# Performance work log

Hardware: AMD Instinct MI355X
Metric: run time of the kernel (lower is better)

## Reference

```python
import jax, jax.numpy as jnp
import numpy as np

B, N, D, H, S = 64, 1000, 512, 8, 20
DK = D // H
TANH_CLIP = 10.0
NEG = -1e9


def setup_inputs() -> dict:
    key = jax.random.key(0)
    k1, k2, k3, k4, k5 = jax.random.split(key, 5)
    embeddings = jax.random.normal(k1, (B, N, D), dtype=jnp.float32)
    q = jax.random.normal(k2, (B, S, D), dtype=jnp.float32)
    # action_mask: True = feasible. Ensure at least one feasible node per row.
    action_mask = jax.random.bernoulli(k3, 0.5, (B, S, N))
    action_mask = action_mask.at[:, :, 0].set(True)
    W_kvl = jax.random.normal(k4, (D, 3 * D), dtype=jnp.float32) * (1.0 / np.sqrt(D))
    W_out = jax.random.normal(k5, (D, D), dtype=jnp.float32) * (1.0 / np.sqrt(D))
    return {"embeddings": embeddings, "q": q, "action_mask": action_mask,
            "W_kvl": W_kvl, "W_out": W_out}


def reference(embeddings, q, action_mask, W_kvl, W_out):
    # _precompute: project node embeddings into glimpse K, V and logit K
    kvl = jnp.einsum('bnd,de->bne', embeddings, W_kvl)  # [B,N,3D]
    glimpse_k, glimpse_v, logit_k = jnp.split(kvl, 3, axis=-1)
    # dynamic embedding is zero (StaticEmbedding for TSP)

    mask = ~action_mask  # True = infeasible, shape [B,S,N]

    # multi-head glimpse attention
    qh = q.reshape(B, S, H, DK)
    kh = glimpse_k.reshape(B, N, H, DK)
    vh = glimpse_v.reshape(B, N, H, DK)
    compat = jnp.einsum('bshd,bnhd->bhsn', qh, kh) / np.sqrt(DK)
    compat = jnp.where(mask[:, None, :, :], NEG, compat)
    attn = jax.nn.softmax(compat, axis=-1)
    heads = jnp.einsum('bhsn,bnhd->bshd', attn, vh).reshape(B, S, D)
    glimpse = jnp.einsum('bsd,de->bse', heads, W_out)  # [B,S,D]

    # pointer logits against logit_k, tanh clipping, mask, log-softmax
    logits = jnp.einsum('bsd,bnd->bsn', glimpse, logit_k) / np.sqrt(D)
    logits = TANH_CLIP * jnp.tanh(logits)
    logits = jnp.where(mask, NEG, logits)
    log_p = jax.nn.log_softmax(logits, axis=-1)  # [B,S,N]

    # rearrange 'b s l -> (s b) l'
    return jnp.swapaxes(log_p, 0, 1).reshape(S * B, N)
```

## Files before the change

### kernel.cpp

```cpp
#include <hip/hip_runtime.h>

#define BB 64
#define NN 1000
#define NP 1024
#define DD 512
#define HH 8
#define SS 20
#define NEGV -1e9f

typedef float v4f __attribute__((ext_vector_type(4)));
typedef short v8s __attribute__((ext_vector_type(8)));
typedef int   v8i __attribute__((ext_vector_type(8)));
typedef int   v4i __attribute__((ext_vector_type(4)));
typedef unsigned char uchar;
typedef unsigned long long ulong_t;

static __device__ __forceinline__ short f2bf(float f) {
    unsigned u = __builtin_bit_cast(unsigned, f);
    u = (u + 0x7fffu + ((u >> 16) & 1u)) >> 16;
    return (short)u;
}
static __device__ __forceinline__ float bf2f(short s) {
    unsigned u = ((unsigned)(unsigned short)s) << 16;
    return __builtin_bit_cast(float, u);
}
static __device__ __forceinline__ uchar f2fp8(float f) {
    return (uchar)(__builtin_amdgcn_cvt_pk_fp8_f32(f, 0.f, 0, false) & 0xff);
}

static __device__ __forceinline__ void gld16(const void* g, void* l) {
    __builtin_amdgcn_global_load_lds(
        (const __attribute__((address_space(1))) void*)(g),
        (__attribute__((address_space(3))) void*)(l),
        16, 0, 0);
}

__global__ void prep(const float* __restrict__ Wkvl, uchar* __restrict__ Wt8,
                     const float* __restrict__ Wout, short* __restrict__ Wot,
                     const float* __restrict__ emb, int* __restrict__ emb8) {
    __shared__ float t[32][33];
    int bid = blockIdx.x, tid = threadIdx.x;
    if (bid < 768) {
        int c0 = (bid % 48) * 32, r0 = (bid / 48) * 32;
        int x = tid & 31, y = tid >> 5;
        for (int k = 0; k < 32; k += 8)
            t[y + k][x] = Wkvl[(long)(r0 + y + k) * 1536 + c0 + x];
        __syncthreads();
        for (int k = 0; k < 32; k += 8)
            Wt8[(long)(c0 + y + k) * 512 + r0 + x] = f2fp8(t[x][y + k]);
    } else if (bid < 1024) {
        int bb = bid - 768;
        int c0 = (bb & 15) * 32, r0 = (bb >> 4) * 32;
        int x = tid & 31, y = tid >> 5;
        for (int k = 0; k < 32; k += 8)
            t[y + k][x] = Wout[(long)(r0 + y + k) * 512 + c0 + x];
        __syncthreads();
        for (int k = 0; k < 32; k += 8)
            Wot[(long)(c0 + y + k) * 512 + r0 + x] = f2bf(t[x][y + k]);
    } else {
        int i = (bid - 1024) * 256 + tid;
        long o = (long)i * 8;
        v4f a = *(const v4f*)(emb + o);
        v4f b = *(const v4f*)(emb + o + 4);
        int lo = __builtin_amdgcn_cvt_pk_fp8_f32(a.x, a.y, 0, false);
        lo = __builtin_amdgcn_cvt_pk_fp8_f32(a.z, a.w, lo, true);
        int hi = __builtin_amdgcn_cvt_pk_fp8_f32(b.x, b.y, 0, false);
        hi = __builtin_amdgcn_cvt_pk_fp8_f32(b.z, b.w, hi, true);
        int2 r; r.x = lo; r.y = hi;
        *(int2*)(emb8 + i * 2) = r;
    }
}

__global__ __launch_bounds__(512) void gemm_kvl(const uchar* __restrict__ emb8,
                                                const uchar* __restrict__ Wt8,
                                                uchar* __restrict__ kvl8) {
    extern __shared__ __align__(16) uchar smem[];
    uchar* As0 = smem;
    uchar* Bs0 = smem + 32768;
    int tid = threadIdx.x;
    int id = blockIdx.x;
    int wgid = (id & 7) * 750 + (id >> 3);
    int m_idx = wgid / 12, n_idx = wgid - m_idx * 12;
    int m0 = m_idx * 128, n0 = n_idx * 128;
    int wid = tid >> 6, lane = tid & 63, quad = lane >> 4, l16 = lane & 15;
    int wm = wid & 1, wn = wid >> 1;
    const uchar* Ag = emb8 + (long)m0 * 512;
    const uchar* Bg = Wt8 + (long)n0 * 512;
    int rsub = lane >> 3;
    int kc = ((lane & 7) ^ rsub) * 16;

    v4f acc[4][2] = {};

    auto stageAB = [&](int bi, int kk) {
        #pragma unroll
        for (int p = 0; p < 2; ++p) {
            int rl = wid * 16 + p * 8;
            gld16(Ag + (long)(rl + rsub) * 512 + kk + kc, As0 + bi * 16384 + rl * 128);
        }
        #pragma unroll
        for (int p = 0; p < 2; ++p) {
            int rl = wid * 16 + p * 8;
            gld16(Bg + (long)(rl + rsub) * 512 + kk + kc, Bs0 + bi * 16384 + rl * 128);
        }
    };
    auto ldfrag = [&](const uchar* base, int row) -> v8i {
        int c0 = (quad * 2) ^ (row & 7);
        v4i lo = *(const v4i*)(base + row * 128 + c0 * 16);
        v4i hi = *(const v4i*)(base + row * 128 + (c0 ^ 1) * 16);
        return __builtin_shufflevector(lo, hi, 0, 1, 2, 3, 4, 5, 6, 7);
    };

    stageAB(0, 0);
    stageAB(1, 128);
    asm volatile("s_waitcnt vmcnt(4)" ::: "memory");
    __builtin_amdgcn_s_barrier();
    __builtin_amdgcn_sched_barrier(0);

    v8i af[4], bf[2];
    #pragma unroll
    for (int t = 0; t < 4; ++t) {
        int cur = t & 1;
        const uchar* ab = As0 + cur * 16384;
        const uchar* bb = Bs0 + cur * 16384;
        #pragma unroll
        for (int i = 0; i < 4; ++i) af[i] = ldfrag(ab, wm * 64 + i * 16 + l16);
        #pragma unroll
        for (int j = 0; j < 2; ++j) bf[j] = ldfrag(bb, wn * 32 + j * 16 + l16);
        __builtin_amdgcn_s_setprio(1);
        #pragma unroll
        for (int i = 0; i < 4; ++i)
            acc[i][0] = __builtin_amdgcn_mfma_scale_f32_16x16x128_f8f6f4(
                af[i], bf[0], acc[i][0], 0, 0, 0, 0x7f7f7f7f, 0, 0x7f7f7f7f);
        __builtin_amdgcn_s_setprio(0);
        asm volatile("s_waitcnt lgkmcnt(0)" ::: "memory");
        __builtin_amdgcn_s_barrier();
        if (t < 2) stageAB(cur, (t + 2) * 128);
        __builtin_amdgcn_s_setprio(1);
        #pragma unroll
        for (int i = 0; i < 4; ++i)
            acc[i][1] = __builtin_amdgcn_mfma_scale_f32_16x16x128_f8f6f4(
                af[i], bf[1], acc[i][1], 0, 0, 0, 0x7f7f7f7f, 0, 0x7f7f7f7f);
        __builtin_amdgcn_s_setprio(0);
        if (t < 3) {
            if (t < 2) asm volatile("s_waitcnt vmcnt(4)" ::: "memory");
            else       asm volatile("s_waitcnt vmcnt(0)" ::: "memory");
            __builtin_amdgcn_s_barrier();
            __builtin_amdgcn_sched_barrier(0);
        }
    }
    __syncthreads();

    short* rp = (short*)smem;
    short* r = rp + wid * (16 * 40);
    int nw = n0 + wn * 32;
    #pragma unroll
    for (int i = 0; i < 4; ++i) {
        #pragma unroll
        for (int jj = 0; jj < 2; ++jj)
            #pragma unroll
            for (int rr = 0; rr < 4; ++rr)
                r[(quad * 4 + rr) * 40 + jj * 16 + l16] = f2bf(acc[i][jj][rr]);
        {
            int rowl = lane >> 2;
            int colc = (lane & 3) * 8;
            v8s val = *(const v8s*)(r + rowl * 40 + colc);
            int lo = __builtin_amdgcn_cvt_pk_fp8_f32(bf2f(val[0]), bf2f(val[1]), 0, false);
            lo = __builtin_amdgcn_cvt_pk_fp8_f32(bf2f(val[2]), bf2f(val[3]), lo, true);
            int hi = __builtin_amdgcn_cvt_pk_fp8_f32(bf2f(val[4]), bf2f(val[5]), 0, false);
            hi = __builtin_amdgcn_cvt_pk_fp8_f32(bf2f(val[6]), bf2f(val[7]), hi, true);
            int2 st; st.x = lo; st.y = hi;
            *(int2*)(kvl8 + (long)(m0 + wm * 64 + i * 16 + rowl) * 1536 +
                     nw + colc) = st;
        }
    }
}

__global__ void pack_kv(const uchar* __restrict__ kvl8, uchar* __restrict__ Kf,
                        uchar* __restrict__ Vf) {
    int bh = blockIdx.x, b = bh >> 3, h = bh & 7;
    int g = blockIdx.y;
    __shared__ uchar Kl[64][72];
    __shared__ uchar VT[64][72];
    int tid = threadIdx.x;
    int node_l = tid >> 2, chunk = (tid & 3) * 16;
    int gn = g * 64 + node_l;
    int ncl = gn < NN ? gn : NN - 1;
    const uchar* rowp = kvl8 + ((long)b * NN + ncl) * 1536 + h * 64;
    *(v4i*)&Kl[node_l][chunk] = *(const v4i*)(rowp + chunk);
    {
        const uchar* vp = rowp + 512 + chunk;
        ulong_t v0 = *(const ulong_t*)(vp);
        ulong_t v1 = *(const ulong_t*)(vp + 8);
        uchar* b0p = (uchar*)&v0; uchar* b1p = (uchar*)&v1;
        #pragma unroll
        for (int j = 0; j < 8; ++j) VT[chunk + j][node_l] = b0p[j];
        #pragma unroll
        for (int j = 0; j < 8; ++j) VT[chunk + 8 + j][node_l] = b1p[j];
    }
    __syncthreads();
    int wid = tid >> 6, lane = tid & 63, l16 = lane & 15, quad = lane >> 4;
    #pragma unroll
    for (int ks = 0; ks < 2; ++ks) {
        ulong_t frag = *(const ulong_t*)&Kl[wid * 16 + l16][ks * 32 + quad * 8];
        *(ulong_t*)(Kf + (((long)bh * 64 + g * 4 + wid) * 2 + ks) * 512 + lane * 8) = frag;
    }
    #pragma unroll
    for (int sub = 0; sub < 2; ++sub) {
        ulong_t frag = *(const ulong_t*)&VT[wid * 16 + l16][sub * 32 + quad * 8];
        *(ulong_t*)(Vf + (((long)bh * 4 + wid) * 32 + g * 2 + sub) * 512 + lane * 8) = frag;
    }
}

#define CST 1036
__global__ __launch_bounds__(512) void attn_fused(const float* __restrict__ q,
                                                  const uchar* __restrict__ Kf,
                                                  const uchar* __restrict__ Vf,
                                                  const int* __restrict__ mask,
                                                  float* __restrict__ heads) {
    int b = blockIdx.x, h = blockIdx.y;
    __shared__ __align__(16) uchar qs[32 * 72];
    __shared__ __align__(16) short cmp[SS * CST];
    int tid = threadIdx.x, wid = tid >> 6, lane = tid & 63, quad = lane >> 4, l16 = lane & 15;
    for (int i = tid; i < 32 * 64; i += 512) {
        int row = i >> 6, col = i & 63;
        float v = (row < SS) ? q[((long)b * SS + row) * DD + h * 64 + col] : 0.f;
        qs[row * 72 + col] = f2fp8(v);
    }
    __syncthreads();
    long af[2][2];
    #pragma unroll
    for (int mt = 0; mt < 2; ++mt)
        #pragma unroll
        for (int ks = 0; ks < 2; ++ks)
            af[mt][ks] = *(const long*)(qs + (mt * 16 + l16) * 72 + ks * 32 + quad * 8);
    const uchar* kfb = Kf + ((long)(b * HH + h) * 64) * 1024;
    for (int t = 0; t < 8; ++t) {
        int nt = wid * 8 + t;
        long b0 = *(const long*)(kfb + (long)nt * 1024 + lane * 8);
        long b1 = *(const long*)(kfb + (long)nt * 1024 + 512 + lane * 8);
        #pragma unroll
        for (int mt = 0; mt < 2; ++mt) {
            v4f a = {};
            a = __builtin_amdgcn_mfma_f32_16x16x32_fp8_fp8(af[mt][0], b0, a, 0, 0, 0);
            a = __builtin_amdgcn_mfma_f32_16x16x32_fp8_fp8(af[mt][1], b1, a, 0, 0, 0);
            #pragma unroll
            for (int r = 0; r < 4; ++r) {
                int s = mt * 16 + quad * 4 + r;
                if (s < SS) cmp[s * CST + nt * 16 + l16] = f2bf(a[r] * 0.125f);
            }
        }
    }
    __syncthreads();
    for (int s = wid; s < SS; s += 8) {
        const int* mr = mask + ((long)b * SS + s) * NN;
        float x[16];
        float mx = NEGV;
        #pragma unroll
        for (int i = 0; i < 16; ++i) {
            int n = lane + 64 * i;
            float v = bf2f(cmp[s * CST + n]);
            bool feas = (n < NN) && (mr[n < NN ? n : 0] != 0);
            x[i] = feas ? v : NEGV;
            mx = fmaxf(mx, x[i]);
        }
        for (int off = 32; off; off >>= 1) mx = fmaxf(mx, __shfl_xor(mx, off));
        float sum = 0.f;
        #pragma unroll
        for (int i = 0; i < 16; ++i) { x[i] = __expf(x[i] - mx); sum += x[i]; }
        for (int off = 32; off; off >>= 1) sum += __shfl_xor(sum, off);
        float inv = 1.0f / sum;
        uchar* pr = (uchar*)cmp + (long)s * (CST * 2);
        #pragma unroll
        for (int i = 0; i < 16; ++i) pr[lane + 64 * i] = f2fp8(x[i] * inv);
    }
    __syncthreads();
    int mt = wid & 1, dt = wid >> 1;
    int srow = mt * 16 + l16; if (srow > SS - 1) srow = SS - 1;
    const uchar* ap = (const uchar*)cmp + (long)srow * (CST * 2) + quad * 8;
    const uchar* vfb = Vf + (((long)(b * HH + h) * 4 + dt) * 32) * 512;
    v4f a0 = {}, a1 = {}, a2 = {}, a3 = {};
    for (int k0s = 0; k0s < 32; k0s += 4) {
        a0 = __builtin_amdgcn_mfma_f32_16x16x32_fp8_fp8(
            *(const long*)(ap + k0s * 32),
            *(const long*)(vfb + (long)k0s * 512 + lane * 8), a0, 0, 0, 0);
        a1 = __builtin_amdgcn_mfma_f32_16x16x32_fp8_fp8(
            *(const long*)(ap + (k0s + 1) * 32),
            *(const long*)(vfb + (long)(k0s + 1) * 512 + lane * 8), a1, 0, 0, 0);
        a2 = __builtin_amdgcn_mfma_f32_16x16x32_fp8_fp8(
            *(const long*)(ap + (k0s + 2) * 32),
            *(const long*)(vfb + (long)(k0s + 2) * 512 + lane * 8), a2, 0, 0, 0);
        a3 = __builtin_amdgcn_mfma_f32_16x16x32_fp8_fp8(
            *(const long*)(ap + (k0s + 3) * 32),
            *(const long*)(vfb + (long)(k0s + 3) * 512 + lane * 8), a3, 0, 0, 0);
    }
    v4f accv = (a0 + a1) + (a2 + a3);
    #pragma unroll
    for (int r = 0; r < 4; ++r) {
        int s = mt * 16 + quad * 4 + r;
        if (s < SS)
            heads[((long)b * SS + s) * DD + h * 64 + dt * 16 + l16] = accv[r];
    }
}

__global__ __launch_bounds__(256) void out_proj(const float* __restrict__ heads,
                                                const short* __restrict__ Wot,
                                                float* __restrict__ glimpse) {
    __shared__ __align__(16) short As[64 * 40], Bs[64 * 40];
    int tid = threadIdx.x;
    int m0 = blockIdx.x * 64, n0 = blockIdx.y * 64;
    int wid = tid >> 6, lane = tid & 63, quad = lane >> 4, l16 = lane & 15;
    int wm = wid & 1, wn = wid >> 1;
    int arow = tid >> 3, akol = (tid & 7) * 4;
    int brow = tid >> 2, bkol = (tid & 3) * 8;
    v4f acc[2][2] = {};
    for (int kk = 0; kk < 512; kk += 32) {
        #pragma unroll
        for (int p = 0; p < 2; ++p) {
            int r = arow + p * 32;
            v4f a = *(const v4f*)(heads + (long)(m0 + r) * 512 + kk + akol);
            short4 s4;
            s4.x = f2bf(a.x); s4.y = f2bf(a.y); s4.z = f2bf(a.z); s4.w = f2bf(a.w);
            *(short4*)(As + r * 40 + akol) = s4;
        }
        *(uint4*)(Bs + brow * 40 + bkol) =
            *(const uint4*)(Wot + (long)(n0 + brow) * 512 + kk + bkol);
        __syncthreads();
        #pragma unroll
        for (int i = 0; i < 2; ++i) {
            v8s af = *(const v8s*)(As + (wm * 32 + i * 16 + l16) * 40 + quad * 8);
            #pragma unroll
            for (int j = 0; j < 2; ++j) {
                v8s bf = *(const v8s*)(Bs + (wn * 32 + j * 16 + l16) * 40 + quad * 8);
                acc[i][j] = __builtin_amdgcn_mfma_f32_16x16x32_bf16(af, bf, acc[i][j], 0, 0, 0);
            }
        }
        __syncthreads();
    }
    #pragma unroll
    for (int i = 0; i < 2; ++i)
        #pragma unroll
        for (int j = 0; j < 2; ++j)
            #pragma unroll
            for (int r = 0; r < 4; ++r)
                glimpse[(long)(m0 + wm * 32 + i * 16 + quad * 4 + r) * 512 +
                        n0 + wn * 32 + j * 16 + l16] = acc[i][j][r];
}

__global__ __launch_bounds__(256) void ptr_logits(const float* __restrict__ glimpse,
                                                  const uchar* __restrict__ kvl8,
                                                  float* __restrict__ logits) {
    int b = blockIdx.x, g = blockIdx.y;
    __shared__ __align__(16) uchar Gs[32 * 520];
    int tid = threadIdx.x;
    #pragma unroll
    for (int it = 0; it < 16; ++it) {
        int e = it * 1024 + tid * 4;
        int row = e >> 9, col = e & 511;
        int pk = 0;
        if (row < SS) {
            v4f a = *(const v4f*)(glimpse + ((long)b * SS + row) * 512 + col);
            pk = __builtin_amdgcn_cvt_pk_fp8_f32(a.x, a.y, 0, false);
            pk = __builtin_amdgcn_cvt_pk_fp8_f32(a.z, a.w, pk, true);
        }
        *(int*)(Gs + row * 520 + col) = pk;
    }
    __syncthreads();
    int wid = tid >> 6, lane = tid & 63, quad = lane >> 4, l16 = lane & 15;
    const float scale = 0.04419417382415922f;
    int nt = g * 4 + wid;
    int n = nt * 16 + l16;
    int ncl = n < NN ? n : NN - 1;
    const uchar* kp = kvl8 + ((long)b * NN + ncl) * 1536 + 1024 + quad * 8;
    v4f acc[2] = {};
    for (int k = 0; k < 16; ++k) {
        long bfr = *(const long*)(kp + k * 32);
        #pragma unroll
        for (int m = 0; m < 2; ++m) {
            long afr = *(const long*)(Gs + (m * 16 + l16) * 520 + k * 32 + quad * 8);
            acc[m] = __builtin_amdgcn_mfma_f32_16x16x32_fp8_fp8(afr, bfr, acc[m], 0, 0, 0);
        }
    }
    #pragma unroll
    for (int m = 0; m < 2; ++m)
        #pragma unroll
        for (int r = 0; r < 4; ++r) {
            int s = m * 16 + quad * 4 + r;
            if (s < SS)
                logits[((long)b * SS + s) * NP + nt * 16 + l16] = acc[m][r] * scale;
        }
}

__global__ __launch_bounds__(256) void logsoftmax_out(const float* __restrict__ logits,
                                                      const int* __restrict__ mask,
                                                      float* __restrict__ out) {
    int row = blockIdx.x;
    int b = row / SS, s = row % SS;
    int tid = threadIdx.x;
    __shared__ float red[8];
    int n0 = tid * 4;
    v4f v = *(const v4f*)(logits + (long)row * NP + n0);
    const int* mr = mask + (long)row * NN;
    float x[4];
    float mx = NEGV;
    #pragma unroll
    for (int j = 0; j < 4; ++j) {
        int n = n0 + j;
        float t = 10.f * tanhf(v[j]);
        bool feas = (n < NN) && (mr[n < NN ? n : 0] != 0);
        x[j] = feas ? t : NEGV;
        mx = fmaxf(mx, x[j]);
    }
    for (int off = 32; off; off >>= 1) mx = fmaxf(mx, __shfl_xor(mx, off));
    int wid = tid >> 6, lane = tid & 63;
    if (lane == 0) red[wid] = mx;
    __syncthreads();
    mx = fmaxf(fmaxf(red[0], red[1]), fmaxf(red[2], red[3]));
    float sum = 0.f;
    #pragma unroll
    for (int j = 0; j < 4; ++j) sum += __expf(x[j] - mx);
    for (int off = 32; off; off >>= 1) sum += __shfl_xor(sum, off);
    __syncthreads();
    if (lane == 0) red[4 + wid] = sum;
    __syncthreads();
    sum = red[4] + red[5] + red[6] + red[7];
    float lse = mx + __logf(sum);
    float* orow = out + ((long)s * BB + b) * NN;
    #pragma unroll
    for (int j = 0; j < 4; ++j) {
        int n = n0 + j;
        if (n < NN) orow[n] = x[j] - lse;
    }
}

extern "C" void kernel_launch(void* const* d_in, const int* in_sizes, int n_in,
                              void* d_out, int out_size, void* d_ws, size_t ws_size,
                              hipStream_t stream) {
    const float* emb  = (const float*)d_in[0];
    const float* q    = (const float*)d_in[1];
    const int*   mask = (const int*)d_in[2];
    const float* Wkvl = (const float*)d_in[3];
    const float* Wout = (const float*)d_in[4];
    float* out = (float*)d_out;

    char* ws = (char*)d_ws;
    uchar* kvl8    = (uchar*)ws; ws += (size_t)64000 * 1536;
    uchar* Vf      = (uchar*)ws; ws += (size_t)512 * 64 * NP;
    uchar* Wt8     = (uchar*)ws; ws += (size_t)1536 * 512;
    uchar* emb8    = (uchar*)ws; ws += (size_t)64000 * 512;
    short* Wot     = (short*)ws; ws += (size_t)512 * 512 * 2;
    float* heads   = (float*)ws; ws += (size_t)BB * SS * DD * 4;
    float* glimpse = (float*)ws; ws += (size_t)BB * SS * DD * 4;
    float* logits  = (float*)ws; ws += (size_t)BB * SS * NP * 4;

    uchar* Kf = Wt8;

    static int s_attr_done = 0;
    if (!s_attr_done) {
        hipFuncSetAttribute(reinterpret_cast<const void*>(gemm_kvl),
                            hipFuncAttributeMaxDynamicSharedMemorySize, 65536);
        s_attr_done = 1;
    }

    prep<<<dim3(1024 + 16000), 256, 0, stream>>>(Wkvl, Wt8, Wout, Wot, emb, (int*)emb8);
    gemm_kvl<<<dim3(6000), 512, 65536, stream>>>(emb8, Wt8, kvl8);
    pack_kv<<<dim3(512, 16), 256, 0, stream>>>(kvl8, Kf, Vf);
    attn_fused<<<dim3(BB, HH), 512, 0, stream>>>(q, Kf, Vf, mask, heads);
    out_proj<<<dim3(20, 8), 256, 0, stream>>>(heads, Wot, glimpse);
    ptr_logits<<<dim3(BB, 16), 256, 0, stream>>>(glimpse, kvl8, logits);
    logsoftmax_out<<<dim3(BB * SS), 256, 0, stream>>>(logits, mask, out);
}
```

Before: 347.3 us.

## Fuse K/V packing into attention kernel, transposing V in shared memory

Removes the separate pack_kv kernel and its Kf/Vf global buffers. The attention kernel now reads K fragments straight from kvl8 and transposes the V slice for its (b,h) into a 64KB LDS buffer before the PV MFMAs. This saves one launch and a global write/read round trip of packed K/V. In exchange it uses about 107KB of dynamic LDS per block, adds 16 extra barriers, and does strided K loads from kvl8 that replace the coalesced packed fragments.

```diff
diff --git a/kernel.cpp b/kernel.cpp
--- a/kernel.cpp
+++ b/kernel.cpp
@@ -175,69 +175,66 @@
     }
 }
 
-__global__ void pack_kv(const uchar* __restrict__ kvl8, uchar* __restrict__ Kf,
-                        uchar* __restrict__ Vf) {
-    int bh = blockIdx.x, b = bh >> 3, h = bh & 7;
-    int g = blockIdx.y;
-    __shared__ uchar Kl[64][72];
-    __shared__ uchar VT[64][72];
-    int tid = threadIdx.x;
-    int node_l = tid >> 2, chunk = (tid & 3) * 16;
-    int gn = g * 64 + node_l;
-    int ncl = gn < NN ? gn : NN - 1;
-    const uchar* rowp = kvl8 + ((long)b * NN + ncl) * 1536 + h * 64;
-    *(v4i*)&Kl[node_l][chunk] = *(const v4i*)(rowp + chunk);
-    {
-        const uchar* vp = rowp + 512 + chunk;
-        ulong_t v0 = *(const ulong_t*)(vp);
-        ulong_t v1 = *(const ulong_t*)(vp + 8);
-        uchar* b0p = (uchar*)&v0; uchar* b1p = (uchar*)&v1;
-        #pragma unroll
-        for (int j = 0; j < 8; ++j) VT[chunk + j][node_l] = b0p[j];
-        #pragma unroll
-        for (int j = 0; j < 8; ++j) VT[chunk + 8 + j][node_l] = b1p[j];
-    }
-    __syncthreads();
-    int wid = tid >> 6, lane = tid & 63, l16 = lane & 15, quad = lane >> 4;
-    #pragma unroll
-    for (int ks = 0; ks < 2; ++ks) {
-        ulong_t frag = *(const ulong_t*)&Kl[wid * 16 + l16][ks * 32 + quad * 8];
-        *(ulong_t*)(Kf + (((long)bh * 64 + g * 4 + wid) * 2 + ks) * 512 + lane * 8) = frag;
-    }
-    #pragma unroll
-    for (int sub = 0; sub < 2; ++sub) {
-        ulong_t frag = *(const ulong_t*)&VT[wid * 16 + l16][sub * 32 + quad * 8];
-        *(ulong_t*)(Vf + (((long)bh * 4 + wid) * 32 + g * 2 + sub) * 512 + lane * 8) = frag;
-    }
-}
-
 #define CST 1036
 __global__ __launch_bounds__(512) void attn_fused(const float* __restrict__ q,
-                                                  const uchar* __restrict__ Kf,
-                                                  const uchar* __restrict__ Vf,
+                                                  const uchar* __restrict__ kvl8,
                                                   const int* __restrict__ mask,
                                                   float* __restrict__ heads) {
+    extern __shared__ __align__(16) uchar asm_[];
+    uchar* qs = asm_;
+    short* cmp = (short*)(asm_ + 2304);
+    uchar* vscr = (uchar*)cmp;
+    uchar* VfL = asm_ + 43744;
     int b = blockIdx.x, h = blockIdx.y;
-    __shared__ __align__(16) uchar qs[32 * 72];
-    __shared__ __align__(16) short cmp[SS * CST];
     int tid = threadIdx.x, wid = tid >> 6, lane = tid & 63, quad = lane >> 4, l16 = lane & 15;
+
     for (int i = tid; i < 32 * 64; i += 512) {
         int row = i >> 6, col = i & 63;
         float v = (row < SS) ? q[((long)b * SS + row) * DD + h * 64 + col] : 0.f;
         qs[row * 72 + col] = f2fp8(v);
     }
-    __syncthreads();
+
+    {
+        int gsub = tid >> 8;
+        int t2 = tid & 255;
+        int node_l = t2 >> 2, chunk = (t2 & 3) * 16;
+        int wid2 = t2 >> 6, lane2 = t2 & 63, l162 = lane2 & 15, quad2 = lane2 >> 4;
+        uchar* VT = vscr + gsub * 4608;
+        for (int gg = 0; gg < 8; ++gg) {
+            int g = gg * 2 + gsub;
+            int gn = g * 64 + node_l;
+            int ncl = gn < NN ? gn : NN - 1;
+            const uchar* vp = kvl8 + ((long)b * NN + ncl) * 1536 + 512 + h * 64 + chunk;
+            ulong_t v0 = *(const ulong_t*)(vp);
+            ulong_t v1 = *(const ulong_t*)(vp + 8);
+            uchar* b0p = (uchar*)&v0; uchar* b1p = (uchar*)&v1;
+            #pragma unroll
+            for (int j = 0; j < 8; ++j) VT[(chunk + j) * 72 + node_l] = b0p[j];
+            #pragma unroll
+            for (int j = 0; j < 8; ++j) VT[(chunk + 8 + j) * 72 + node_l] = b1p[j];
+            __syncthreads();
+            #pragma unroll
+            for (int sub = 0; sub < 2; ++sub) {
+                ulong_t frag = *(const ulong_t*)&VT[(wid2 * 16 + l162) * 72 + sub * 32 + quad2 * 8];
+                *(ulong_t*)(VfL + ((wid2 * 32) + (g * 2 + sub)) * 512 + lane2 * 8) = frag;
+            }
+            __syncthreads();
+        }
+    }
+
     long af[2][2];
     #pragma unroll
     for (int mt = 0; mt < 2; ++mt)
         #pragma unroll
         for (int ks = 0; ks < 2; ++ks)
             af[mt][ks] = *(const long*)(qs + (mt * 16 + l16) * 72 + ks * 32 + quad * 8);
-    const uchar* kfb = Kf + ((long)(b * HH + h) * 64) * 1024;
     for (int t = 0; t < 8; ++t) {
         int nt = wid * 8 + t;
-        long b0 = *(const long*)(kfb + (long)nt * 1024 + lane * 8);
-        long b1 = *(const long*)(kfb + (long)nt * 1024 + 512 + lane * 8);
+        int n = nt * 16 + l16;
+        int nc = n < NN ? n : NN - 1;
+        const uchar* kp = kvl8 + ((long)b * NN + nc) * 1536 + h * 64 + quad * 8;
+        long b0 = *(const long*)kp;
+        long b1 = *(const long*)(kp + 32);
         #pragma unroll
         for (int mt = 0; mt < 2; ++mt) {
             v4f a = {};
@@ -277,21 +274,21 @@
     int mt = wid & 1, dt = wid >> 1;
     int srow = mt * 16 + l16; if (srow > SS - 1) srow = SS - 1;
     const uchar* ap = (const uchar*)cmp + (long)srow * (CST * 2) + quad * 8;
-    const uchar* vfb = Vf + (((long)(b * HH + h) * 4 + dt) * 32) * 512;
+    const uchar* vfb = VfL + dt * 32 * 512;
     v4f a0 = {}, a1 = {}, a2 = {}, a3 = {};
     for (int k0s = 0; k0s < 32; k0s += 4) {
         a0 = __builtin_amdgcn_mfma_f32_16x16x32_fp8_fp8(
             *(const long*)(ap + k0s * 32),
-            *(const long*)(vfb + (long)k0s * 512 + lane * 8), a0, 0, 0, 0);
+            *(const long*)(vfb + k0s * 512 + lane * 8), a0, 0, 0, 0);
         a1 = __builtin_amdgcn_mfma_f32_16x16x32_fp8_fp8(
             *(const long*)(ap + (k0s + 1) * 32),
-            *(const long*)(vfb + (long)(k0s + 1) * 512 + lane * 8), a1, 0, 0, 0);
+            *(const long*)(vfb + (k0s + 1) * 512 + lane * 8), a1, 0, 0, 0);
         a2 = __builtin_amdgcn_mfma_f32_16x16x32_fp8_fp8(
             *(const long*)(ap + (k0s + 2) * 32),
-            *(const long*)(vfb + (long)(k0s + 2) * 512 + lane * 8), a2, 0, 0, 0);
+            *(const long*)(vfb + (k0s + 2) * 512 + lane * 8), a2, 0, 0, 0);
         a3 = __builtin_amdgcn_mfma_f32_16x16x32_fp8_fp8(
             *(const long*)(ap + (k0s + 3) * 32),
-            *(const long*)(vfb + (long)(k0s + 3) * 512 + lane * 8), a3, 0, 0, 0);
+            *(const long*)(vfb + (k0s + 3) * 512 + lane * 8), a3, 0, 0, 0);
     }
     v4f accv = (a0 + a1) + (a2 + a3);
     #pragma unroll
@@ -444,7 +441,6 @@
 
     char* ws = (char*)d_ws;
     uchar* kvl8    = (uchar*)ws; ws += (size_t)64000 * 1536;
-    uchar* Vf      = (uchar*)ws; ws += (size_t)512 * 64 * NP;
     uchar* Wt8     = (uchar*)ws; ws += (size_t)1536 * 512;
     uchar* emb8    = (uchar*)ws; ws += (size_t)64000 * 512;
     short* Wot     = (short*)ws; ws += (size_t)512 * 512 * 2;
@@ -452,19 +448,18 @@
     float* glimpse = (float*)ws; ws += (size_t)BB * SS * DD * 4;
     float* logits  = (float*)ws; ws += (size_t)BB * SS * NP * 4;
 
-    uchar* Kf = Wt8;
-
     static int s_attr_done = 0;
     if (!s_attr_done) {
         hipFuncSetAttribute(reinterpret_cast<const void*>(gemm_kvl),
                             hipFuncAttributeMaxDynamicSharedMemorySize, 65536);
+        hipFuncSetAttribute(reinterpret_cast<const void*>(attn_fused),
+                            hipFuncAttributeMaxDynamicSharedMemorySize, 109312);
         s_attr_done = 1;
     }
 
     prep<<<dim3(1024 + 16000), 256, 0, stream>>>(Wkvl, Wt8, Wout, Wot, emb, (int*)emb8);
     gemm_kvl<<<dim3(6000), 512, 65536, stream>>>(emb8, Wt8, kvl8);
-    pack_kv<<<dim3(512, 16), 256, 0, stream>>>(kvl8, Kf, Vf);
-    attn_fused<<<dim3(BB, HH), 512, 0, stream>>>(q, Kf, Vf, mask, heads);
+    attn_fused<<<dim3(BB, HH), 512, 109312, stream>>>(q, kvl8, mask, heads);
     out_proj<<<dim3(20, 8), 256, 0, stream>>>(heads, Wot, glimpse);
     ptr_logits<<<dim3(BB, 16), 256, 0, stream>>>(glimpse, kvl8, logits);
     logsoftmax_out<<<dim3(BB * SS), 256, 0, stream>>>(logits, mask, out);
```

Result: faster. 335.5 us (-3.4%).
